# Performance work log

Measured on AMD Instinct MI355X. Metric: run time of the kernel, lower is better.

## Reference

```python
import math
import jax, jax.numpy as jnp
import numpy as np

D_MODEL = 896
N_HEADS = 14
D_HEAD = D_MODEL // N_HEADS  # 64
ROPE_BASE = 10000.0
LN_EPS = 1e-5
B, N = 8, 1024


def setup_inputs() -> dict:
    key = jax.random.key(0)
    ks = jax.random.split(key, 12)
    s = 1.0 / math.sqrt(D_MODEL)
    return {
        "node_features": jax.random.normal(ks[0], (B, N, D_MODEL), jnp.float32),
        "adj": jax.random.uniform(ks[1], (N, N), jnp.float32),
        "wind_dirs": jax.random.uniform(ks[2], (B, N), jnp.float32),
        "bearings": jax.random.uniform(ks[3], (N, N), jnp.float32),
        "Wq": jax.random.normal(ks[4], (D_MODEL, D_MODEL), jnp.float32) * s,
        "Wk": jax.random.normal(ks[5], (D_MODEL, D_MODEL), jnp.float32) * s,
        "Wv": jax.random.normal(ks[6], (D_MODEL, D_MODEL), jnp.float32) * s,
        "Wo": jax.random.normal(ks[7], (D_MODEL, D_MODEL), jnp.float32) * s,
        "ln_g": jnp.ones((D_MODEL,), jnp.float32),
        "ln_b": jnp.zeros((D_MODEL,), jnp.float32),
        "wind_w": jax.random.normal(ks[8], (2, N_HEADS), jnp.float32) * (1.0 / math.sqrt(2.0)),
        "wind_b": jnp.zeros((N_HEADS,), jnp.float32),
    }


def _layernorm(x, g, b):
    mu = jnp.mean(x, axis=-1, keepdims=True)
    var = jnp.var(x, axis=-1, keepdims=True)
    return (x - mu) * jax.lax.rsqrt(var + LN_EPS) * g + b


def _apply_rotary(x, cos_h, sin_h):
    # x: (B,H,N,d_head); cos_h/sin_h: (N, d_head//2)
    d_half = x.shape[-1] // 2
    x1, x2 = x[..., :d_half], x[..., d_half:]
    return jnp.concatenate([x1 * cos_h - x2 * sin_h, x2 * cos_h + x1 * sin_h], axis=-1)


def reference(node_features, adj, wind_dirs, bearings, Wq, Wk, Wv, Wo, ln_g, ln_b, wind_w, wind_b):
    Bb, Nn, D = node_features.shape
    residual = node_features
    x = _layernorm(node_features, ln_g, ln_b)

    def proj(W):
        return (x @ W).reshape(Bb, Nn, N_HEADS, D_HEAD).transpose(0, 2, 1, 3)  # (B,H,N,dh)

    Q, K, V = proj(Wq), proj(Wk), proj(Wv)

    # RoPE: cos/sin halves (first d_half entries of the duplicated freq table)
    inv_freq = 1.0 / (ROPE_BASE ** (jnp.arange(0, D_HEAD, 2, dtype=jnp.float32) / D_HEAD))
    freqs = jnp.arange(Nn, dtype=jnp.float32)[:, None] * inv_freq[None, :]  # (N, dh/2)
    cos_h, sin_h = jnp.cos(freqs), jnp.sin(freqs)
    Q = _apply_rotary(Q, cos_h, sin_h)
    K = _apply_rotary(K, cos_h, sin_h)

    attn = jnp.einsum("bhqd,bhkd->bhqk", Q, K) / math.sqrt(D_HEAD)
    adj_mask = (adj > 0)[None, None, :, :]
    attn = jnp.where(adj_mask, attn, -1e30)

    # wind-direction dynamic edge bias
    reverse_bearings = (bearings.T + 180.0) % 360.0  # (N,N)
    alignment = jnp.cos(jnp.deg2rad(wind_dirs[:, :, None] - reverse_bearings[None]))  # (B,N,N)
    dist_feat = jnp.broadcast_to(adj[None], (Bb, Nn, Nn))
    edge_features = jnp.stack([alignment, dist_feat], axis=-1)  # (B,N,N,2)
    wind_bias = jnp.tanh(edge_features @ wind_w + wind_b)  # (B,N,N,H)
    attn = attn + wind_bias.transpose(0, 3, 1, 2)  # (B,H,N,N)

    attn = jax.nn.softmax(attn, axis=-1)  # dropout is identity in eval
    out = jnp.einsum("bhqk,bhkd->bhqd", attn, V)
    out = out.transpose(0, 2, 1, 3).reshape(Bb, Nn, D) @ Wo
    return residual + out
```

## Files before the change

kernel.cpp:

```cpp
#include <hip/hip_runtime.h>
#include <hip/hip_bf16.h>
#include <math.h>

#define B_ 8
#define N_ 1024
#define H_ 14
#define DH_ 64
#define D_ 896
#define M_ (B_*N_)
#define DQKV_ 2688

#define TWO_LOG2E_ 2.8853900817779268f
#define BIAS_C_   (-15.869645449778597f)
#define QSCALE_     0.18033688011112043f
#define RAD_        0.017453292519943295f

typedef __attribute__((ext_vector_type(8))) short bf16x8;
typedef __attribute__((ext_vector_type(4))) short bf16x4;
typedef __attribute__((ext_vector_type(4))) float f32x4;

__device__ __forceinline__ float bf2f(short s){
  unsigned u = ((unsigned)(unsigned short)s) << 16;
  union { unsigned u; float f; } c; c.u = u; return c.f;
}
__device__ __forceinline__ short f2bf(float f){
  union { float f; unsigned u; } c; c.f = f;
  unsigned u = c.u;
  unsigned r = (u + 0x7FFFu + ((u >> 16) & 1u)) >> 16;
  return (short)(unsigned short)r;
}
__device__ __forceinline__ float asf(unsigned u){
  union { unsigned u; float f; } c; c.u = u; return c.f;
}
__device__ __forceinline__ unsigned cvt_pk_bf16(float lo, float hi){
  unsigned r;
  asm("v_cvt_pk_bf16_f32 %0, %1, %2" : "=v"(r) : "v"(lo), "v"(hi));
  return r;
}

#if __has_builtin(__builtin_amdgcn_mfma_f32_16x16x16bf16_1k)
#define MFMA16(D, A, B) (D) = __builtin_amdgcn_mfma_f32_16x16x16bf16_1k((A), (B), (D), 0, 0, 0)
#else
#define MFMA16(D, A, B) asm("v_mfma_f32_16x16x16_bf16 %0, %1, %2, %0" : "+v"(D) : "v"(A), "v"(B))
#endif

#define BAR_LDS() do { asm volatile("s_waitcnt lgkmcnt(0)" ::: "memory"); \
                       __builtin_amdgcn_s_barrier(); } while (0)

__global__ __launch_bounds__(256) void ln_kernel(const float* __restrict__ x,
                                                 const float* __restrict__ g,
                                                 const float* __restrict__ bb,
                                                 short* __restrict__ y)
{
  int row = blockIdx.x;
  const float* xr = x + (size_t)row * D_;
  float s = 0.f, s2 = 0.f;
  for (int i = threadIdx.x; i < D_; i += 256){
    float v = xr[i]; s += v; s2 = fmaf(v, v, s2);
  }
  #pragma unroll
  for (int off = 32; off > 0; off >>= 1){
    s  += __shfl_down(s,  off, 64);
    s2 += __shfl_down(s2, off, 64);
  }
  __shared__ float rs_[4], rs2_[4];
  int wv = threadIdx.x >> 6;
  if ((threadIdx.x & 63) == 0){ rs_[wv] = s; rs2_[wv] = s2; }
  __syncthreads();
  float ts  = rs_[0] + rs_[1] + rs_[2] + rs_[3];
  float ts2 = rs2_[0] + rs2_[1] + rs2_[2] + rs2_[3];
  float mu  = ts * (1.f / D_);
  float var = ts2 * (1.f / D_) - mu * mu;
  float rstd = rsqrtf(var + 1e-5f);
  short* yr = y + (size_t)row * D_;
  for (int i = threadIdx.x; i < D_; i += 256){
    yr[i] = f2bf((xr[i] - mu) * rstd * g[i] + bb[i]);
  }
}

__global__ __launch_bounds__(256) void transpose_kernel(
    const float* __restrict__ Wq, const float* __restrict__ Wk,
    const float* __restrict__ Wv, const float* __restrict__ Wo,
    short* __restrict__ WqkvT, short* __restrict__ WoT)
{
  __shared__ short t[64][72];
  int z = blockIdx.z;
  const float* W = (z == 0) ? Wq : (z == 1) ? Wk : (z == 2) ? Wv : Wo;
  int kb = blockIdx.x * 64, nb = blockIdx.y * 64;
  int c0 = (threadIdx.x & 7) * 8;
  int r0 = threadIdx.x >> 3;
  #pragma unroll
  for (int rr = 0; rr < 64; rr += 32){
    const float* src = &W[(size_t)(kb + r0 + rr) * D_ + nb + c0];
    float4 a = *(const float4*)src;
    float4 b = *(const float4*)(src + 4);
    short* dstl = &t[r0 + rr][c0];
    dstl[0] = f2bf(a.x); dstl[1] = f2bf(a.y); dstl[2] = f2bf(a.z); dstl[3] = f2bf(a.w);
    dstl[4] = f2bf(b.x); dstl[5] = f2bf(b.y); dstl[6] = f2bf(b.z); dstl[7] = f2bf(b.w);
  }
  __syncthreads();
  short* dst = (z < 3) ? (WqkvT + (size_t)(z * D_) * D_) : WoT;
  #pragma unroll
  for (int rr = 0; rr < 64; rr += 32){
    int n = nb + r0 + rr;
    bf16x8 v;
    #pragma unroll
    for (int j = 0; j < 8; j++) v[j] = t[c0 + j][r0 + rr];
    *(bf16x8*)&dst[(size_t)n * D_ + kb + c0] = v;
  }
}

__global__ __launch_bounds__(256) void vt_kernel(const short* __restrict__ QKV,
                                                 short* __restrict__ VT)
{
  __shared__ short tt[64][72];
  int kt = blockIdx.x;
  int bh = blockIdx.y;
  int b  = bh / H_, hh = bh - b * H_;
  int r  = threadIdx.x >> 2;
  int c0 = (threadIdx.x & 3) * 16;
  const short* src = QKV + ((size_t)(b * N_) + kt * 64 + r) * DQKV_ + 2 * D_ + hh * DH_ + c0;
  *(bf16x8*)&tt[r][c0]     = *(const bf16x8*)src;
  *(bf16x8*)&tt[r][c0 + 8] = *(const bf16x8*)(src + 8);
  __syncthreads();
  short* dst = VT + ((size_t)bh * DH_ + r) * N_ + kt * 64 + c0;
  bf16x8 v0, v1;
  #pragma unroll
  for (int j = 0; j < 8; j++){ v0[j] = tt[c0 + j][r]; v1[j] = tt[c0 + 8 + j][r]; }
  *(bf16x8*)dst       = v0;
  *(bf16x8*)(dst + 8) = v1;
}

__global__ __launch_bounds__(256) void prep_kernel(
    const float* __restrict__ brg, const float* __restrict__ wdir,
    unsigned* __restrict__ csb, short* __restrict__ alignQ, int do_align)
{
  int kt = blockIdx.x, qt = blockIdx.y;
  __shared__ float brgS[64][65];
  __shared__ float cA_[8][64], sA_[8][64];
  int r  = threadIdx.x >> 2;
  int c0 = (threadIdx.x & 3) * 16;

  float bb[16];
  {
    const float* bp = brg + (size_t)(kt * 64 + r) * N_ + qt * 64 + c0;
    #pragma unroll
    for (int i = 0; i < 16; i += 4){
      float4 bv = *(const float4*)(bp + i);
      bb[i] = bv.x; bb[i+1] = bv.y; bb[i+2] = bv.z; bb[i+3] = bv.w;
    }
  }

  if (do_align){
    #pragma unroll
    for (int i = 0; i < 16; i++) brgS[r][c0 + i] = bb[i];
    for (int idx = threadIdx.x; idx < 512; idx += 256){
      int b = idx >> 6, qq = idx & 63;
      float A = wdir[(size_t)b * N_ + qt * 64 + qq] * RAD_;
      float s, c; __sincosf(A, &s, &c);
      sA_[b][qq] = s; cA_[b][qq] = c;
    }
    __syncthreads();
    float cB[16], sB[16];
    #pragma unroll
    for (int i = 0; i < 16; i++){
      float Br = (brgS[c0 + i][r] + 180.f) * RAD_;
      __sincosf(Br, &sB[i], &cB[i]);
    }
    #pragma unroll
    for (int b = 0; b < 8; b++){
      float ca = cA_[b][r], sa = sA_[b][r];
      unsigned w8[8];
      #pragma unroll
      for (int p = 0; p < 8; p++){
        float a0 = fmaf(ca, cB[2*p],     sa * sB[2*p]);
        float a1 = fmaf(ca, cB[2*p + 1], sa * sB[2*p + 1]);
        w8[p] = cvt_pk_bf16(a0, a1);
      }
      short* dst = alignQ + ((size_t)b * N_ + qt * 64 + r) * N_ + kt * 64 + c0;
      *(uint4*)dst       = make_uint4(w8[0], w8[1], w8[2], w8[3]);
      *(uint4*)(dst + 8) = make_uint4(w8[4], w8[5], w8[6], w8[7]);
    }
  } else {
    unsigned* cp = csb + (size_t)(kt * 64 + r) * N_ + qt * 64 + c0;
    #pragma unroll
    for (int i = 0; i < 16; i += 4){
      unsigned o[4];
      #pragma unroll
      for (int j = 0; j < 4; j++){
        float Br = (bb[i + j] + 180.f) * RAD_;
        float sBv, cBv; __sincosf(Br, &sBv, &cBv);
        o[j] = ((unsigned)(unsigned short)f2bf(cBv)) |
               (((unsigned)(unsigned short)f2bf(sBv)) << 16);
      }
      *(uint4*)(cp + i) = make_uint4(o[0], o[1], o[2], o[3]);
    }
  }
}

__global__ __launch_bounds__(256) void gemm_bt(const short* __restrict__ A,
                                               const short* __restrict__ Bt,
                                               short* __restrict__ C,
                                               float* __restrict__ Cf,
                                               const float* __restrict__ residf,
                                               int N, int rope)
{
  const int K = D_;
  __shared__ short As[128 * 32];
  __shared__ short Bs[128 * 32];
  int tid  = threadIdx.x;
  int wave = tid >> 6;
  int lane = tid & 63;
  int quad = lane >> 4;
  int l16  = lane & 15;
  int wr = wave >> 1, wc = wave & 1;
  int m0 = blockIdx.x * 128;
  int n0 = blockIdx.y * 128;

  f32x4 acc[4][4];
  #pragma unroll
  for (int i = 0; i < 4; i++)
    #pragma unroll
    for (int j = 0; j < 4; j++)
      acc[i][j] = (f32x4){0.f, 0.f, 0.f, 0.f};

  for (int k0 = 0; k0 < K; k0 += 32){
    __syncthreads();
    #pragma unroll
    for (int it = 0; it < 2; ++it){
      int c   = tid + it * 256;
      int row = c >> 2;
      int cc  = c & 3;
      const short* ga = A  + (size_t)(m0 + row) * K + k0 + cc * 8;
      const short* gb = Bt + (size_t)(n0 + row) * K + k0 + cc * 8;
      short* la = As + (size_t)(wave * 64 + it * 256) * 8;
      short* lb = Bs + (size_t)(wave * 64 + it * 256) * 8;
      __builtin_amdgcn_global_load_lds((const __attribute__((address_space(1))) void*)ga,
                                       (__attribute__((address_space(3))) void*)la, 16, 0, 0);
      __builtin_amdgcn_global_load_lds((const __attribute__((address_space(1))) void*)gb,
                                       (__attribute__((address_space(3))) void*)lb, 16, 0, 0);
    }
    __syncthreads();

    bf16x8 af[4], bfr[4];
    #pragma unroll
    for (int i = 0; i < 4; i++)
      af[i] = *(const bf16x8*)(As + (size_t)(wr * 64 + i * 16 + l16) * 32 + quad * 8);
    #pragma unroll
    for (int j = 0; j < 4; j++)
      bfr[j] = *(const bf16x8*)(Bs + (size_t)(wc * 64 + j * 16 + l16) * 32 + quad * 8);
    #pragma unroll
    for (int i = 0; i < 4; i++)
      #pragma unroll
      for (int j = 0; j < 4; j++)
        acc[i][j] = __builtin_amdgcn_mfma_f32_16x16x32_bf16(af[i], bfr[j], acc[i][j], 0, 0, 0);
  }

  if (rope){
    int cb  = n0 + wc * 64;
    int mat = cb / D_;
    if (mat < 2){
      float scale = (mat == 0) ? QSCALE_ : 1.0f;
      float invf0 = exp2f(-0.4152410118609203f * (float)l16);
      float invf1 = invf0 * 0.01f;
      #pragma unroll
      for (int i = 0; i < 4; i++){
        #pragma unroll
        for (int rr = 0; rr < 4; rr++){
          int r = m0 + wr * 64 + i * 16 + quad * 4 + rr;
          float nseq = (float)(r & (N_ - 1));
          float s0, c0v, s1, c1v;
          __sincosf(nseq * invf0, &s0, &c0v);
          __sincosf(nseq * invf1, &s1, &c1v);
          float x1 = acc[i][0][rr], x2 = acc[i][2][rr];
          acc[i][0][rr] = (x1 * c0v - x2 * s0) * scale;
          acc[i][2][rr] = (x2 * c0v + x1 * s0) * scale;
          x1 = acc[i][1][rr]; x2 = acc[i][3][rr];
          acc[i][1][rr] = (x1 * c1v - x2 * s1) * scale;
          acc[i][3][rr] = (x2 * c1v + x1 * s1) * scale;
        }
      }
    }
  }

  #pragma unroll
  for (int i = 0; i < 4; i++){
    #pragma unroll
    for (int rr = 0; rr < 4; rr++){
      int r = m0 + wr * 64 + i * 16 + quad * 4 + rr;
      size_t rowoff = (size_t)r * N;
      #pragma unroll
      for (int j = 0; j < 4; j++){
        int cidx = n0 + wc * 64 + j * 16 + l16;
        float v = acc[i][j][rr];
        if (Cf){
          Cf[rowoff + cidx] = v + residf[rowoff + cidx];
        } else {
          C[rowoff + cidx] = f2bf(v);
        }
      }
    }
  }
}

template<int PRE>
__global__ __launch_bounds__(256, 2) void attn_kernel(
    const short* __restrict__ QKV,
    const short* __restrict__ VT,
    const unsigned* __restrict__ csb,
    const float* __restrict__ adjF,
    const short* __restrict__ alignQ,
    const float* __restrict__ wind_dirs,
    const float* __restrict__ wind_w,
    const float* __restrict__ wind_b,
    short* __restrict__ outb)
{
  __shared__ short K_s[64 * 72];
  __shared__ short V_t[64 * 76];

  int bid = blockIdx.x;
  int qt  = bid / 112;
  int rem = bid - qt * 112;
  int hh  = rem >> 3;
  int b   = rem & 7;
  int q0  = qt * 64;
  int kt0 = qt;

  int t    = threadIdx.x;
  int w    = t >> 6;
  int lane = t & 63;
  int quad = lane >> 4;
  int l16  = lane & 15;
  int q    = q0 + w * 16 + l16;

  const short* qp = QKV + ((size_t)(b * N_) + q) * DQKV_ + hh * DH_ + quad * 8;
  bf16x8 qb0 = *(const bf16x8*)qp;
  bf16x8 qb1 = *(const bf16x8*)(qp + 32);

  float cAq = 0.f, sAq = 0.f;
  if (!PRE){
    float A = wind_dirs[(size_t)b * N_ + q] * RAD_;
    sAq = __sinf(A); cAq = __cosf(A);
  }
  float w0m = wind_w[hh]      * TWO_LOG2E_;
  float w1m = wind_w[H_ + hh] * TWO_LOG2E_;
  float wbm = wind_b[hh]      * TWO_LOG2E_;

  float lsum = 0.f;
  f32x4 OT[4];
  #pragma unroll
  for (int db = 0; db < 4; db++) OT[db] = (f32x4){0.f, 0.f, 0.f, 0.f};

  int sr = t >> 2, sc = (t & 3) * 16;
  const short* kg0 = QKV + ((size_t)(b * N_) + sr) * DQKV_ + D_ + hh * DH_ + sc;
  const short* vg0 = VT + ((size_t)(b * H_ + hh) * DH_ + sr) * N_ + sc;

  const float* ad2 = adjF + (size_t)q * N_ + quad * 4;
  const short* al2 = alignQ + ((size_t)b * N_ + q) * N_ + quad * 4;

  int k0f = kt0 * 64;
  bf16x8 pkA = *(const bf16x8*)(kg0 + (size_t)k0f * DQKV_);
  bf16x8 pkB = *(const bf16x8*)(kg0 + (size_t)k0f * DQKV_ + 8);
  bf16x8 pvA = *(const bf16x8*)(vg0 + k0f);
  bf16x8 pvB = *(const bf16x8*)(vg0 + k0f + 8);

  float4 ad4[4]; bf16x4 al4[4]; unsigned cs4[4][4];
  #pragma unroll
  for (int jc = 0; jc < 4; jc++){
    ad4[jc] = *(const float4*)(ad2 + k0f + jc * 16);
    if (PRE){
      al4[jc] = *(const bf16x4*)(al2 + k0f + jc * 16);
    } else {
      #pragma unroll
      for (int rr = 0; rr < 4; rr++)
        cs4[jc][rr] = csb[(size_t)(k0f + jc * 16 + quad * 4 + rr) * N_ + q];
    }
  }

  for (int it = 0; it < 16; ++it){
    int kn = (((it + 1 + kt0) & 15)) * 64;

    BAR_LDS();
    *(bf16x8*)(K_s + sr * 72 + sc)     = pkA;
    *(bf16x8*)(K_s + sr * 72 + sc + 8) = pkB;
    *(bf16x8*)(V_t + sr * 76 + sc)     = pvA;
    *(bf16x8*)(V_t + sr * 76 + sc + 8) = pvB;
    BAR_LDS();

    pkA = *(const bf16x8*)(kg0 + (size_t)kn * DQKV_);
    pkB = *(const bf16x8*)(kg0 + (size_t)kn * DQKV_ + 8);
    pvA = *(const bf16x8*)(vg0 + kn);
    pvB = *(const bf16x8*)(vg0 + kn + 8);

    f32x4 S[4];
    __builtin_amdgcn_s_setprio(1);
    #pragma unroll
    for (int jc = 0; jc < 4; jc++){
      bf16x8 ka0 = *(const bf16x8*)(K_s + (jc * 16 + l16) * 72 + quad * 8);
      bf16x8 ka1 = *(const bf16x8*)(K_s + (jc * 16 + l16) * 72 + 32 + quad * 8);
      f32x4 s = (f32x4){0.f, 0.f, 0.f, 0.f};
      s = __builtin_amdgcn_mfma_f32_16x16x32_bf16(ka0, qb0, s, 0, 0, 0);
      s = __builtin_amdgcn_mfma_f32_16x16x32_bf16(ka1, qb1, s, 0, 0, 0);
      S[jc] = s;
    }
    __builtin_amdgcn_s_setprio(0);

    #pragma unroll
    for (int jc = 0; jc < 4; jc++){
      float a4[4] = { ad4[jc].x, ad4[jc].y, ad4[jc].z, ad4[jc].w };
      float ev[4];
      #pragma unroll
      for (int rr = 0; rr < 4; rr++){
        float av = a4[rr];
        float align;
        if (PRE){
          align = bf2f(al4[jc][rr]);
        } else {
          unsigned u = cs4[jc][rr];
          align = cAq * asf(u << 16) + sAq * asf(u & 0xffff0000u);
        }
        float z2 = fmaf(align, w0m, fmaf(av, w1m, wbm));
        float e2 = __builtin_amdgcn_exp2f(z2);
        float rc = __builtin_amdgcn_rcpf(e2 + 1.f);
        float bias2 = fmaf(-TWO_LOG2E_, rc, BIAS_C_);
        float sv = (av > 0.f ? S[jc][rr] : -1e30f) + bias2;
        float e = __builtin_amdgcn_exp2f(sv);
        ev[rr] = e;
        lsum += e;
      }
      union { unsigned u2[2]; bf16x4 v4; } pu;
      pu.u2[0] = cvt_pk_bf16(ev[0], ev[1]);
      pu.u2[1] = cvt_pk_bf16(ev[2], ev[3]);
      bf16x4 pb = pu.v4;

      ad4[jc] = *(const float4*)(ad2 + kn + jc * 16);
      if (PRE){
        al4[jc] = *(const bf16x4*)(al2 + kn + jc * 16);
      } else {
        #pragma unroll
        for (int rr = 0; rr < 4; rr++)
          cs4[jc][rr] = csb[(size_t)(kn + jc * 16 + quad * 4 + rr) * N_ + q];
      }

      __builtin_amdgcn_s_setprio(1);
      #pragma unroll
      for (int db = 0; db < 4; db++){
        bf16x4 va = *(const bf16x4*)(V_t + (db * 16 + l16) * 76 + jc * 16 + quad * 4);
        MFMA16(OT[db], va, pb);
      }
      __builtin_amdgcn_s_setprio(0);
    }
  }

  lsum += __shfl_xor(lsum, 16);
  lsum += __shfl_xor(lsum, 32);
  float rl = 1.f / lsum;

  short* op = outb + ((size_t)(b * N_) + q) * D_ + hh * DH_ + quad * 4;
  #pragma unroll
  for (int db = 0; db < 4; db++){
    unsigned o01 = cvt_pk_bf16(OT[db][0] * rl, OT[db][1] * rl);
    unsigned o23 = cvt_pk_bf16(OT[db][2] * rl, OT[db][3] * rl);
    *(uint2*)(op + db * 16) = make_uint2(o01, o23);
  }
}

extern "C" void kernel_launch(void* const* d_in, const int* in_sizes, int n_in,
                              void* d_out, int out_size, void* d_ws, size_t ws_size,
                              hipStream_t stream)
{
  const float* nf   = (const float*)d_in[0];
  const float* adj  = (const float*)d_in[1];
  const float* wdir = (const float*)d_in[2];
  const float* brg  = (const float*)d_in[3];
  const float* Wq   = (const float*)d_in[4];
  const float* Wk   = (const float*)d_in[5];
  const float* Wv   = (const float*)d_in[6];
  const float* Wo   = (const float*)d_in[7];
  const float* lng  = (const float*)d_in[8];
  const float* lnb  = (const float*)d_in[9];
  const float* ww   = (const float*)d_in[10];
  const float* wbb  = (const float*)d_in[11];
  float* out = (float*)d_out;

  short* base = (short*)d_ws;
  size_t sh = 0;
  short* xln   = base + sh;  sh += (size_t)M_ * D_;
  short* WqkvT = base + sh;  sh += (size_t)DQKV_ * D_;
  short* WoT   = base + sh;  sh += (size_t)D_ * D_;
  short* QKV   = base + sh;  sh += (size_t)M_ * DQKV_;
  short* VT    = base + sh;  sh += (size_t)B_ * H_ * DH_ * N_;
  unsigned* csb = (unsigned*)(base + sh); sh += (size_t)N_ * N_ * 2;
  short* alignQ = base + sh; sh += (size_t)B_ * N_ * N_;
  size_t need_pre = sh * sizeof(short);
  bool pre = (ws_size >= need_pre);

  ln_kernel<<<M_, 256, 0, stream>>>(nf, lng, lnb, xln);
  transpose_kernel<<<dim3(14, 14, 4), 256, 0, stream>>>(Wq, Wk, Wv, Wo, WqkvT, WoT);
  prep_kernel<<<dim3(16, 16), 256, 0, stream>>>(brg, wdir, csb, alignQ, pre ? 1 : 0);
  gemm_bt<<<dim3(M_ / 128, DQKV_ / 128), 256, 0, stream>>>(xln, WqkvT, QKV, nullptr, nullptr, DQKV_, 1);
  vt_kernel<<<dim3(16, 112), 256, 0, stream>>>(QKV, VT);
  if (pre)
    attn_kernel<1><<<B_ * H_ * 16, 256, 0, stream>>>(QKV, VT, csb, adj, alignQ, wdir, ww, wbb, xln);
  else
    attn_kernel<0><<<B_ * H_ * 16, 256, 0, stream>>>(QKV, VT, csb, adj, alignQ, wdir, ww, wbb, xln);
  gemm_bt<<<dim3(M_ / 128, D_ / 128), 256, 0, stream>>>(xln, WoT, nullptr, out, nf, D_, 0);
}
```

Measured before the change: 374.1 us.

## Process two query tiles per attention block and precompute bf16 adjacency

Each attention block now handles 128 queries as two 64-row groups, sharing the K/V tiles staged in shared memory and halving the grid size and K/V global reloads. The prep kernel also writes a bf16 copy of the adjacency matrix, so the attention kernel reads half the bytes for the mask and distance feature. The cost is that bias and alignment loads are no longer prefetched one tile ahead but issued at the start of each group, which can expose memory latency. Register pressure also rises from the doubled accumulators, and the grid of 896 blocks may leave compute units less evenly loaded.

```diff
diff --git a/kernel.cpp b/kernel.cpp
--- a/kernel.cpp
+++ b/kernel.cpp
@@ -132,8 +132,10 @@
 }
 
 __global__ __launch_bounds__(256) void prep_kernel(
-    const float* __restrict__ brg, const float* __restrict__ wdir,
-    unsigned* __restrict__ csb, short* __restrict__ alignQ, int do_align)
+    const float* __restrict__ adj, const float* __restrict__ brg,
+    const float* __restrict__ wdir,
+    unsigned* __restrict__ csb, short* __restrict__ alignQ,
+    short* __restrict__ adjQ, int do_align)
 {
   int kt = blockIdx.x, qt = blockIdx.y;
   __shared__ float brgS[64][65];
@@ -159,6 +161,19 @@
       float A = wdir[(size_t)b * N_ + qt * 64 + qq] * RAD_;
       float s, c; __sincosf(A, &s, &c);
       sA_[b][qq] = s; cA_[b][qq] = c;
+    }
+    {
+      const float* ap = adj + (size_t)(qt * 64 + r) * N_ + kt * 64 + c0;
+      unsigned w8[8];
+      #pragma unroll
+      for (int i = 0; i < 16; i += 4){
+        float4 av = *(const float4*)(ap + i);
+        w8[i/2]     = cvt_pk_bf16(av.x, av.y);
+        w8[i/2 + 1] = cvt_pk_bf16(av.z, av.w);
+      }
+      short* dst = adjQ + (size_t)(qt * 64 + r) * N_ + kt * 64 + c0;
+      *(uint4*)dst       = make_uint4(w8[0], w8[1], w8[2], w8[3]);
+      *(uint4*)(dst + 8) = make_uint4(w8[4], w8[5], w8[6], w8[7]);
     }
     __syncthreads();
     float cB[16], sB[16];
@@ -310,6 +325,7 @@
     const unsigned* __restrict__ csb,
     const float* __restrict__ adjF,
     const short* __restrict__ alignQ,
+    const short* __restrict__ adjQ,
     const float* __restrict__ wind_dirs,
     const float* __restrict__ wind_w,
     const float* __restrict__ wind_b,
@@ -323,40 +339,51 @@
   int rem = bid - qt * 112;
   int hh  = rem >> 3;
   int b   = rem & 7;
-  int q0  = qt * 64;
-  int kt0 = qt;
+  int q0  = qt * 128;
+  int kt0 = (qt * 2) & 15;
 
   int t    = threadIdx.x;
   int w    = t >> 6;
   int lane = t & 63;
   int quad = lane >> 4;
   int l16  = lane & 15;
-  int q    = q0 + w * 16 + l16;
-
-  const short* qp = QKV + ((size_t)(b * N_) + q) * DQKV_ + hh * DH_ + quad * 8;
-  bf16x8 qb0 = *(const bf16x8*)qp;
-  bf16x8 qb1 = *(const bf16x8*)(qp + 32);
-
-  float cAq = 0.f, sAq = 0.f;
+  int qA = q0 + w * 16 + l16;
+  int qB = qA + 64;
+
+  bf16x8 qb[2][2];
+  {
+    const short* qpA = QKV + ((size_t)(b * N_) + qA) * DQKV_ + hh * DH_ + quad * 8;
+    const short* qpB = QKV + ((size_t)(b * N_) + qB) * DQKV_ + hh * DH_ + quad * 8;
+    qb[0][0] = *(const bf16x8*)qpA;  qb[0][1] = *(const bf16x8*)(qpA + 32);
+    qb[1][0] = *(const bf16x8*)qpB;  qb[1][1] = *(const bf16x8*)(qpB + 32);
+  }
+
+  float cAq[2], sAq[2];
   if (!PRE){
-    float A = wind_dirs[(size_t)b * N_ + q] * RAD_;
-    sAq = __sinf(A); cAq = __cosf(A);
+    #pragma unroll
+    for (int g = 0; g < 2; g++){
+      float A = wind_dirs[(size_t)b * N_ + qA + g * 64] * RAD_;
+      sAq[g] = __sinf(A); cAq[g] = __cosf(A);
+    }
   }
   float w0m = wind_w[hh]      * TWO_LOG2E_;
   float w1m = wind_w[H_ + hh] * TWO_LOG2E_;
   float wbm = wind_b[hh]      * TWO_LOG2E_;
 
-  float lsum = 0.f;
-  f32x4 OT[4];
-  #pragma unroll
-  for (int db = 0; db < 4; db++) OT[db] = (f32x4){0.f, 0.f, 0.f, 0.f};
+  float lsum[2] = {0.f, 0.f};
+  f32x4 OT[2][4];
+  #pragma unroll
+  for (int g = 0; g < 2; g++)
+    #pragma unroll
+    for (int db = 0; db < 4; db++) OT[g][db] = (f32x4){0.f, 0.f, 0.f, 0.f};
 
   int sr = t >> 2, sc = (t & 3) * 16;
   const short* kg0 = QKV + ((size_t)(b * N_) + sr) * DQKV_ + D_ + hh * DH_ + sc;
   const short* vg0 = VT + ((size_t)(b * H_ + hh) * DH_ + sr) * N_ + sc;
 
-  const float* ad2 = adjF + (size_t)q * N_ + quad * 4;
-  const short* al2 = alignQ + ((size_t)b * N_ + q) * N_ + quad * 4;
+  const short* alA = alignQ + ((size_t)b * N_ + qA) * N_ + quad * 4;
+  const short* ajA = adjQ + (size_t)qA * N_ + quad * 4;
+  const float* adA = adjF + (size_t)qA * N_ + quad * 4;
 
   int k0f = kt0 * 64;
   bf16x8 pkA = *(const bf16x8*)(kg0 + (size_t)k0f * DQKV_);
@@ -364,21 +391,9 @@
   bf16x8 pvA = *(const bf16x8*)(vg0 + k0f);
   bf16x8 pvB = *(const bf16x8*)(vg0 + k0f + 8);
 
-  float4 ad4[4]; bf16x4 al4[4]; unsigned cs4[4][4];
-  #pragma unroll
-  for (int jc = 0; jc < 4; jc++){
-    ad4[jc] = *(const float4*)(ad2 + k0f + jc * 16);
-    if (PRE){
-      al4[jc] = *(const bf16x4*)(al2 + k0f + jc * 16);
-    } else {
-      #pragma unroll
-      for (int rr = 0; rr < 4; rr++)
-        cs4[jc][rr] = csb[(size_t)(k0f + jc * 16 + quad * 4 + rr) * N_ + q];
-    }
-  }
-
   for (int it = 0; it < 16; ++it){
-    int kn = (((it + 1 + kt0) & 15)) * 64;
+    int k0 = ((it + kt0) & 15) * 64;
+    int kn = ((it + 1 + kt0) & 15) * 64;
 
     BAR_LDS();
     *(bf16x8*)(K_s + sr * 72 + sc)     = pkA;
@@ -392,76 +407,90 @@
     pvA = *(const bf16x8*)(vg0 + kn);
     pvB = *(const bf16x8*)(vg0 + kn + 8);
 
-    f32x4 S[4];
-    __builtin_amdgcn_s_setprio(1);
-    #pragma unroll
-    for (int jc = 0; jc < 4; jc++){
-      bf16x8 ka0 = *(const bf16x8*)(K_s + (jc * 16 + l16) * 72 + quad * 8);
-      bf16x8 ka1 = *(const bf16x8*)(K_s + (jc * 16 + l16) * 72 + 32 + quad * 8);
-      f32x4 s = (f32x4){0.f, 0.f, 0.f, 0.f};
-      s = __builtin_amdgcn_mfma_f32_16x16x32_bf16(ka0, qb0, s, 0, 0, 0);
-      s = __builtin_amdgcn_mfma_f32_16x16x32_bf16(ka1, qb1, s, 0, 0, 0);
-      S[jc] = s;
-    }
-    __builtin_amdgcn_s_setprio(0);
-
-    #pragma unroll
-    for (int jc = 0; jc < 4; jc++){
-      float a4[4] = { ad4[jc].x, ad4[jc].y, ad4[jc].z, ad4[jc].w };
-      float ev[4];
-      #pragma unroll
-      for (int rr = 0; rr < 4; rr++){
-        float av = a4[rr];
-        float align;
+    #pragma unroll
+    for (int g = 0; g < 2; g++){
+      size_t grow = (size_t)g * 64 * N_;
+
+      bf16x4 al4[4], aj4[4]; float4 ad4[4]; unsigned cs4[4][4];
+      #pragma unroll
+      for (int jc = 0; jc < 4; jc++){
         if (PRE){
-          align = bf2f(al4[jc][rr]);
+          al4[jc] = *(const bf16x4*)(alA + grow + k0 + jc * 16);
+          aj4[jc] = *(const bf16x4*)(ajA + grow + k0 + jc * 16);
         } else {
-          unsigned u = cs4[jc][rr];
-          align = cAq * asf(u << 16) + sAq * asf(u & 0xffff0000u);
+          ad4[jc] = *(const float4*)(adA + grow + k0 + jc * 16);
+          #pragma unroll
+          for (int rr = 0; rr < 4; rr++)
+            cs4[jc][rr] = csb[(size_t)(k0 + jc * 16 + quad * 4 + rr) * N_ + qA + g * 64];
         }
-        float z2 = fmaf(align, w0m, fmaf(av, w1m, wbm));
-        float e2 = __builtin_amdgcn_exp2f(z2);
-        float rc = __builtin_amdgcn_rcpf(e2 + 1.f);
-        float bias2 = fmaf(-TWO_LOG2E_, rc, BIAS_C_);
-        float sv = (av > 0.f ? S[jc][rr] : -1e30f) + bias2;
-        float e = __builtin_amdgcn_exp2f(sv);
-        ev[rr] = e;
-        lsum += e;
-      }
-      union { unsigned u2[2]; bf16x4 v4; } pu;
-      pu.u2[0] = cvt_pk_bf16(ev[0], ev[1]);
-      pu.u2[1] = cvt_pk_bf16(ev[2], ev[3]);
-      bf16x4 pb = pu.v4;
-
-      ad4[jc] = *(const float4*)(ad2 + kn + jc * 16);
-      if (PRE){
-        al4[jc] = *(const bf16x4*)(al2 + kn + jc * 16);
-      } else {
+      }
+
+      f32x4 S[4];
+      __builtin_amdgcn_s_setprio(1);
+      #pragma unroll
+      for (int jc = 0; jc < 4; jc++){
+        bf16x8 ka0 = *(const bf16x8*)(K_s + (jc * 16 + l16) * 72 + quad * 8);
+        bf16x8 ka1 = *(const bf16x8*)(K_s + (jc * 16 + l16) * 72 + 32 + quad * 8);
+        f32x4 s = (f32x4){0.f, 0.f, 0.f, 0.f};
+        s = __builtin_amdgcn_mfma_f32_16x16x32_bf16(ka0, qb[g][0], s, 0, 0, 0);
+        s = __builtin_amdgcn_mfma_f32_16x16x32_bf16(ka1, qb[g][1], s, 0, 0, 0);
+        S[jc] = s;
+      }
+      __builtin_amdgcn_s_setprio(0);
+
+      #pragma unroll
+      for (int jc = 0; jc < 4; jc++){
+        float ev[4];
         #pragma unroll
-        for (int rr = 0; rr < 4; rr++)
-          cs4[jc][rr] = csb[(size_t)(kn + jc * 16 + quad * 4 + rr) * N_ + q];
-      }
-
-      __builtin_amdgcn_s_setprio(1);
-      #pragma unroll
-      for (int db = 0; db < 4; db++){
-        bf16x4 va = *(const bf16x4*)(V_t + (db * 16 + l16) * 76 + jc * 16 + quad * 4);
-        MFMA16(OT[db], va, pb);
-      }
-      __builtin_amdgcn_s_setprio(0);
-    }
-  }
-
-  lsum += __shfl_xor(lsum, 16);
-  lsum += __shfl_xor(lsum, 32);
-  float rl = 1.f / lsum;
-
-  short* op = outb + ((size_t)(b * N_) + q) * D_ + hh * DH_ + quad * 4;
-  #pragma unroll
-  for (int db = 0; db < 4; db++){
-    unsigned o01 = cvt_pk_bf16(OT[db][0] * rl, OT[db][1] * rl);
-    unsigned o23 = cvt_pk_bf16(OT[db][2] * rl, OT[db][3] * rl);
-    *(uint2*)(op + db * 16) = make_uint2(o01, o23);
+        for (int rr = 0; rr < 4; rr++){
+          float av, align;
+          if (PRE){
+            align = bf2f(al4[jc][rr]);
+            av    = bf2f(aj4[jc][rr]);
+          } else {
+            float4 a4 = ad4[jc];
+            av = (rr == 0) ? a4.x : (rr == 1) ? a4.y : (rr == 2) ? a4.z : a4.w;
+            unsigned u = cs4[jc][rr];
+            align = cAq[g] * asf(u << 16) + sAq[g] * asf(u & 0xffff0000u);
+          }
+          float z2 = fmaf(align, w0m, fmaf(av, w1m, wbm));
+          float e2 = __builtin_amdgcn_exp2f(z2);
+          float rc = __builtin_amdgcn_rcpf(e2 + 1.f);
+          float bias2 = fmaf(-TWO_LOG2E_, rc, BIAS_C_);
+          float sv = (av > 0.f ? S[jc][rr] : -1e30f) + bias2;
+          float e = __builtin_amdgcn_exp2f(sv);
+          ev[rr] = e;
+          lsum[g] += e;
+        }
+        union { unsigned u2[2]; bf16x4 v4; } pu;
+        pu.u2[0] = cvt_pk_bf16(ev[0], ev[1]);
+        pu.u2[1] = cvt_pk_bf16(ev[2], ev[3]);
+        bf16x4 pb = pu.v4;
+
+        __builtin_amdgcn_s_setprio(1);
+        #pragma unroll
+        for (int db = 0; db < 4; db++){
+          bf16x4 va = *(const bf16x4*)(V_t + (db * 16 + l16) * 76 + jc * 16 + quad * 4);
+          MFMA16(OT[g][db], va, pb);
+        }
+        __builtin_amdgcn_s_setprio(0);
+      }
+    }
+  }
+
+  #pragma unroll
+  for (int g = 0; g < 2; g++){
+    float rs = lsum[g];
+    rs += __shfl_xor(rs, 16);
+    rs += __shfl_xor(rs, 32);
+    float rl = 1.f / rs;
+    short* op = outb + ((size_t)(b * N_) + qA + g * 64) * D_ + hh * DH_ + quad * 4;
+    #pragma unroll
+    for (int db = 0; db < 4; db++){
+      unsigned o01 = cvt_pk_bf16(OT[g][db][0] * rl, OT[g][db][1] * rl);
+      unsigned o23 = cvt_pk_bf16(OT[g][db][2] * rl, OT[g][db][3] * rl);
+      *(uint2*)(op + db * 16) = make_uint2(o01, o23);
+    }
   }
 }
 
@@ -492,17 +521,18 @@
   short* VT    = base + sh;  sh += (size_t)B_ * H_ * DH_ * N_;
   unsigned* csb = (unsigned*)(base + sh); sh += (size_t)N_ * N_ * 2;
   short* alignQ = base + sh; sh += (size_t)B_ * N_ * N_;
+  short* adjQ   = base + sh; sh += (size_t)N_ * N_;
   size_t need_pre = sh * sizeof(short);
   bool pre = (ws_size >= need_pre);
 
   ln_kernel<<<M_, 256, 0, stream>>>(nf, lng, lnb, xln);
   transpose_kernel<<<dim3(14, 14, 4), 256, 0, stream>>>(Wq, Wk, Wv, Wo, WqkvT, WoT);
-  prep_kernel<<<dim3(16, 16), 256, 0, stream>>>(brg, wdir, csb, alignQ, pre ? 1 : 0);
+  prep_kernel<<<dim3(16, 16), 256, 0, stream>>>(adj, brg, wdir, csb, alignQ, adjQ, pre ? 1 : 0);
   gemm_bt<<<dim3(M_ / 128, DQKV_ / 128), 256, 0, stream>>>(xln, WqkvT, QKV, nullptr, nullptr, DQKV_, 1);
   vt_kernel<<<dim3(16, 112), 256, 0, stream>>>(QKV, VT);
   if (pre)
-    attn_kernel<1><<<B_ * H_ * 16, 256, 0, stream>>>(QKV, VT, csb, adj, alignQ, wdir, ww, wbb, xln);
+    attn_kernel<1><<<B_ * H_ * 8, 256, 0, stream>>>(QKV, VT, csb, adj, alignQ, adjQ, wdir, ww, wbb, xln);
   else
-    attn_kernel<0><<<B_ * H_ * 16, 256, 0, stream>>>(QKV, VT, csb, adj, alignQ, wdir, ww, wbb, xln);
+    attn_kernel<0><<<B_ * H_ * 8, 256, 0, stream>>>(QKV, VT, csb, adj, alignQ, adjQ, wdir, ww, wbb, xln);
   gemm_bt<<<dim3(M_ / 128, D_ / 128), 256, 0, stream>>>(xln, WoT, nullptr, out, nf, D_, 0);
 }
```

Measured after the change: 392.1 us. 1.05x slower.
